# Performance work log

Hardware: AMD Instinct MI355X
Metric: run time of the kernel (lower is better)

Reference implementation:

```python
import jax, jax.numpy as jnp
import numpy as np
import math

HEADS = 16
HIDDEN = 2048
D_K = HIDDEN // HEADS
BATCH = 2
SEQ = 2048
ROPE_THETA = 10000.0


def make_freqs_cis(seq_len, d_k, theta=ROPE_THETA):
    # Llama rotary frequencies; returned as (seq, d_k//2, 2) = (cos, sin)
    inv_freq = 1.0 / (theta ** (np.arange(0, d_k, 2, dtype=np.float32) / d_k))
    t = np.arange(seq_len, dtype=np.float32)
    ang = np.outer(t, inv_freq)  # (seq, d_k//2)
    return jnp.asarray(np.stack([np.cos(ang), np.sin(ang)], axis=-1))


def setup_inputs() -> dict:
    key = jax.random.key(0)
    ks = jax.random.split(key, 5)
    scale = 1.0 / math.sqrt(HIDDEN)
    return {
        "x": jax.random.normal(ks[0], (BATCH, SEQ, HIDDEN), dtype=jnp.float32),
        "freqs_cis": make_freqs_cis(SEQ, D_K),
        "wq": jax.random.normal(ks[1], (HIDDEN, HIDDEN), dtype=jnp.float32) * scale,
        "wk": jax.random.normal(ks[2], (HIDDEN, HIDDEN), dtype=jnp.float32) * scale,
        "wv": jax.random.normal(ks[3], (HIDDEN, HIDDEN), dtype=jnp.float32) * scale,
        "wo": jax.random.normal(ks[4], (HIDDEN, HIDDEN), dtype=jnp.float32) * scale,
    }


def _apply_rope(t, cos, sin):
    # t: (B, S, h, d_k); cos/sin: (1, S, 1, d_k//2)
    B, S, h, dk = t.shape
    tp = t.reshape(B, S, h, dk // 2, 2)
    t0, t1 = tp[..., 0], tp[..., 1]
    r0 = t0 * cos - t1 * sin
    r1 = t0 * sin + t1 * cos
    return jnp.stack([r0, r1], axis=-1).reshape(B, S, h, dk)


def reference(x, freqs_cis, wq, wk, wv, wo):
    B, S, H = x.shape
    h, dk = HEADS, H // HEADS
    # nn.Linear(bias=False): y = x @ W.T
    q = (x @ wq.T).reshape(B, S, h, dk)
    k = (x @ wk.T).reshape(B, S, h, dk)
    v = (x @ wv.T).reshape(B, S, h, dk)
    cos = freqs_cis[None, :, None, :, 0]
    sin = freqs_cis[None, :, None, :, 1]
    q = _apply_rope(q, cos, sin)
    k = _apply_rope(k, cos, sin)
    # (B, h, S, dk)
    q = q.transpose(0, 2, 1, 3)
    k = k.transpose(0, 2, 1, 3)
    v = v.transpose(0, 2, 1, 3)
    scores = jnp.einsum("bhqd,bhkd->bhqk", q, k) / math.sqrt(dk)
    causal = jnp.tril(jnp.ones((S, S), dtype=bool))
    scores = jnp.where(causal[None, None], scores, -jnp.inf)
    attn = jax.nn.softmax(scores, axis=-1)
    out = jnp.einsum("bhqk,bhkd->bhqd", attn, v)
    out = out.transpose(0, 2, 1, 3).reshape(B, S, H)
    return out @ wo.T
```

## Files before the change

kernel.cpp:

```cpp
#include <hip/hip_runtime.h>

#define SEQ 2048
#define HID 2048
#define NH 16
#define DK 128
#define NTOK 4096

typedef __bf16 bf16x8 __attribute__((ext_vector_type(8)));
typedef float f32x4 __attribute__((ext_vector_type(4)));
typedef unsigned int u32x4 __attribute__((ext_vector_type(4)));

__device__ __forceinline__ unsigned short f2bf(float f) {
  unsigned int u = __builtin_bit_cast(unsigned int, f);
  u += 0x7fffu + ((u >> 16) & 1u);
  return (unsigned short)(u >> 16);
}
__device__ __forceinline__ float bf2f(unsigned int lo16) {
  return __builtin_bit_cast(float, lo16 << 16);
}

__device__ __forceinline__ void async_cp16(const void* g, void* l) {
  __builtin_amdgcn_global_load_lds(
      (__attribute__((address_space(1))) void*)const_cast<void*>(g),
      (__attribute__((address_space(3))) void*)l, 16, 0, 0);
}

__global__ void convert_all_kernel(const float* __restrict__ x,
                                   const float* __restrict__ wq,
                                   const float* __restrict__ wk,
                                   const float* __restrict__ wv,
                                   const float* __restrict__ wo,
                                   unsigned short* __restrict__ xb,
                                   unsigned short* __restrict__ wqb,
                                   unsigned short* __restrict__ wkb,
                                   unsigned short* __restrict__ wvb,
                                   unsigned short* __restrict__ wob) {
  const int bid = blockIdx.x;
  const float* src;
  unsigned short* dst;
  int base;
  if (bid < 8192) {
    src = x; dst = xb; base = bid;
  } else {
    const int t = (bid - 8192) >> 12;
    base = (bid - 8192) & 4095;
    src = (t == 0) ? wq : (t == 1) ? wk : (t == 2) ? wv : wo;
    dst = (t == 0) ? wqb : (t == 1) ? wkb : (t == 2) ? wvb : wob;
  }
  const int i = base * 256 + threadIdx.x;
  float4 v = ((const float4*)src)[i];
  ushort4 o;
  o.x = f2bf(v.x); o.y = f2bf(v.y); o.z = f2bf(v.z); o.w = f2bf(v.w);
  ((ushort4*)dst)[i] = o;
}

template<bool F32OUT>
__global__ __launch_bounds__(256, 3)
void gemm_bt_kernel(const unsigned short* __restrict__ A,
                    const unsigned short* __restrict__ B0,
                    const unsigned short* __restrict__ B1,
                    const unsigned short* __restrict__ B2,
                    unsigned short* __restrict__ O0,
                    unsigned short* __restrict__ O1,
                    unsigned short* __restrict__ O2,
                    float* __restrict__ Of,
                    const float* __restrict__ fc) {
  __shared__ alignas(16) unsigned short As[128 * 64];
  __shared__ alignas(16) unsigned short Bs[128 * 64];

  const int bx = blockIdx.x, by = blockIdx.y;
  const unsigned short* B;
  unsigned short* Ob = nullptr;
  int sel = 0, col0;
  if (F32OUT) {
    B = B0;
    col0 = bx * 128;
  } else {
    sel = bx >> 4;
    B = (sel == 0) ? B0 : (sel == 1) ? B1 : B2;
    Ob = (sel == 0) ? O0 : (sel == 1) ? O1 : O2;
    col0 = (bx & 15) * 128;
  }
  const int row0 = by * 128;

  const int tid = threadIdx.x;
  const int wave = tid >> 6, lane = tid & 63;
  const int quad = lane >> 4, r = lane & 15;
  const int wm = wave >> 1, wn = wave & 1;
  const int jbase = wave * 256 + lane;

  f32x4 acc[4][4] = {};

  for (int k0 = 0; k0 < HID; k0 += 64) {
    for (int t = 0; t < 4; ++t) {
      const int j = jbase + t * 64;
      const int m = j >> 3;
      const int gc = (j & 7) ^ (m & 7);
      async_cp16(A + (size_t)(row0 + m) * HID + k0 + gc * 8, As + j * 8);
      async_cp16(B + (size_t)(col0 + m) * HID + k0 + gc * 8, Bs + j * 8);
    }
    __syncthreads();
    for (int kk = 0; kk < 2; ++kk) {
      bf16x8 af[4], bfr[4];
      for (int mt = 0; mt < 4; ++mt) {
        const int m = wm * 64 + mt * 16 + r;
        const int slot = (kk * 4 + quad) ^ (m & 7);
        af[mt] = __builtin_bit_cast(bf16x8, *(const u32x4*)(As + m * 64 + slot * 8));
      }
      for (int nt = 0; nt < 4; ++nt) {
        const int n = wn * 64 + nt * 16 + r;
        const int slot = (kk * 4 + quad) ^ (n & 7);
        bfr[nt] = __builtin_bit_cast(bf16x8, *(const u32x4*)(Bs + n * 64 + slot * 8));
      }
      for (int mt = 0; mt < 4; ++mt)
        for (int nt = 0; nt < 4; ++nt)
          acc[mt][nt] = __builtin_amdgcn_mfma_f32_16x16x32_bf16(
              af[mt], bfr[nt], acc[mt][nt], 0, 0, 0);
    }
    __syncthreads();
  }

  if (!F32OUT && sel == 2) {
    for (int mt = 0; mt < 4; ++mt) {
      const int row = row0 + wm * 64 + mt * 16 + quad * 4;
      const int b = row >> 11, s = row & (SEQ - 1);
      for (int nt = 0; nt < 4; ++nt) {
        const int col = col0 + wn * 64 + nt * 16 + r;
        ushort4 pk;
        pk.x = f2bf(acc[mt][nt][0]);
        pk.y = f2bf(acc[mt][nt][1]);
        pk.z = f2bf(acc[mt][nt][2]);
        pk.w = f2bf(acc[mt][nt][3]);
        *(ushort4*)(Ob + ((size_t)(b * HID + col)) * SEQ + s) = pk;
      }
    }
    return;
  }

  if (!F32OUT) {
    const float qs = (sel == 0) ? 0.08838834764831845f : 1.0f;
    for (int mt = 0; mt < 4; ++mt) {
      const int row = row0 + wm * 64 + mt * 16 + quad * 4;
      for (int nt = 0; nt < 4; ++nt) {
        const int col = col0 + wn * 64 + nt * 16 + r;
        const int d = (wn * 64 + nt * 16 + r) >> 1;
        for (int v = 0; v < 4; ++v) {
          const int s = (row + v) & (SEQ - 1);
          const float2 cs = *(const float2*)(fc + s * 128 + 2 * d);
          const float val = acc[mt][nt][v];
          const float par = __shfl_xor(val, 1, 64);
          const float res = (r & 1) ? (par * cs.y + val * cs.x)
                                    : (val * cs.x - par * cs.y);
          Ob[(size_t)(row + v) * HID + col] = f2bf(res * qs);
        }
      }
    }
    return;
  }

  for (int mt = 0; mt < 4; ++mt) {
    const int row = row0 + wm * 64 + mt * 16 + quad * 4;
    for (int nt = 0; nt < 4; ++nt) {
      const int col = col0 + wn * 64 + nt * 16 + r;
      for (int v = 0; v < 4; ++v)
        Of[(size_t)(row + v) * HID + col] = acc[mt][nt][v];
    }
  }
}

__global__ __launch_bounds__(256, 2)
void flash_attn_kernel(const unsigned short* __restrict__ Qb,
                       const unsigned short* __restrict__ Kb,
                       const unsigned short* __restrict__ VtG,
                       unsigned short* __restrict__ Ob) {
  __shared__ alignas(16) unsigned short KsA[64 * 128];
  __shared__ alignas(16) unsigned short KsB[64 * 128];
  __shared__ alignas(16) unsigned short VsA[128 * 64];
  __shared__ alignas(16) unsigned short VsB[128 * 64];
  __shared__ alignas(16) unsigned short Ps[4][16 * 64];

  const int bx = blockIdx.x, bh = blockIdx.y;
  const int tid = threadIdx.x, wave = tid >> 6, lane = tid & 63;
  const int quad = lane >> 4, r = lane & 15;
  const int tokbase = (bh >> 4) * SEQ;
  const int h = bh & 15;

  const u32x4 onesv = {0x3F803F80u, 0x3F803F80u, 0x3F803F80u, 0x3F803F80u};

  auto stage = [&](int kt, unsigned short* Ks, unsigned short* Vs) {
    for (int t = 0; t < 4; ++t) {
      const int j = t * 256 + tid;
      const int n = j >> 4, slot = j & 15;
      const int gc = (slot & 8) | ((slot & 7) ^ (n & 7));
      async_cp16(Kb + (size_t)(tokbase + kt * 64 + n) * HID + h * DK + gc * 8,
                 Ks + j * 8);
    }
    for (int t = 0; t < 4; ++t) {
      const int j = t * 256 + tid;
      const int d = j >> 3, slot = j & 7;
      const int gc = slot ^ (d & 7);
      async_cp16(VtG + ((size_t)(bh * DK + d)) * SEQ + kt * 64 + gc * 8,
                 Vs + j * 8);
    }
  };

  for (int phase = 0; phase < 2; ++phase) {
    const int qt = phase ? (31 - bx) : bx;
    const int q0 = qt * 64;

    u32x4 qf[4];
    {
      const unsigned short* qrow =
          Qb + (size_t)(tokbase + q0 + wave * 16 + r) * HID + h * DK;
      for (int kk = 0; kk < 4; ++kk)
        qf[kk] = *(const u32x4*)(qrow + kk * 32 + quad * 8);
    }

    f32x4 o[8] = {};
    float m_i[4], l_i[4];
    for (int v = 0; v < 4; ++v) { m_i[v] = -__builtin_inff(); l_i[v] = 0.f; }

    auto body = [&](const unsigned short* Ks, const unsigned short* Vs, int kt) {
      f32x4 s[4];
      for (int nt = 0; nt < 4; ++nt) {
        f32x4 a = {};
        const int n = nt * 16 + r;
        for (int kk = 0; kk < 4; ++kk) {
          const int c = kk * 4 + quad;
          const int slot = (c & 8) | ((c & 7) ^ (r & 7));
          u32x4 bkf = *(const u32x4*)(Ks + n * 128 + slot * 8);
          a = __builtin_amdgcn_mfma_f32_16x16x32_bf16(
              __builtin_bit_cast(bf16x8, qf[kk]),
              __builtin_bit_cast(bf16x8, bkf), a, 0, 0, 0);
        }
        s[nt] = a;
      }

      if (kt == qt) {
        const int qrow_g = q0 + wave * 16 + quad * 4;
        for (int nt = 0; nt < 4; ++nt) {
          const int col = kt * 64 + nt * 16 + r;
          for (int v = 0; v < 4; ++v)
            if (col > qrow_g + v) s[nt][v] = -__builtin_inff();
        }
      }

      float mx[4];
      for (int v = 0; v < 4; ++v)
        mx[v] = fmaxf(fmaxf(s[0][v], s[1][v]), fmaxf(s[2][v], s[3][v]));
      for (int off = 1; off < 16; off <<= 1)
        for (int v = 0; v < 4; ++v)
          mx[v] = fmaxf(mx[v], __shfl_xor(mx[v], off, 64));

      float alpha[4];
      for (int v = 0; v < 4; ++v) {
        const float mnew = fmaxf(m_i[v], mx[v]);
        alpha[v] = __expf(m_i[v] - mnew);
        m_i[v] = mnew;
      }

      unsigned short* ps = &Ps[wave][0];
      for (int nt = 0; nt < 4; ++nt) {
        const int chunk = nt * 2 + (r >> 3);
        for (int v = 0; v < 4; ++v) {
          const float p = __expf(s[nt][v] - m_i[v]);
          const int row = quad * 4 + v;
          const int slot = chunk ^ (row & 7);
          ps[row * 64 + slot * 8 + (r & 7)] = f2bf(p);
        }
      }
      for (int dt = 0; dt < 8; ++dt)
        for (int v = 0; v < 4; ++v)
          o[dt][v] *= alpha[v];
      __asm__ volatile("" ::: "memory");

      f32x4 rsacc = {};
      for (int kk2 = 0; kk2 < 2; ++kk2) {
        const int c = kk2 * 4 + quad;
        const int aslot = c ^ (r & 7);
        u32x4 pa = *(const u32x4*)(ps + r * 64 + aslot * 8);
        rsacc = __builtin_amdgcn_mfma_f32_16x16x32_bf16(
            __builtin_bit_cast(bf16x8, pa),
            __builtin_bit_cast(bf16x8, onesv), rsacc, 0, 0, 0);
        for (int dt = 0; dt < 8; ++dt) {
          const int d = dt * 16 + r;
          const int bslot = c ^ (d & 7);
          u32x4 bv = *(const u32x4*)(Vs + d * 64 + bslot * 8);
          o[dt] = __builtin_amdgcn_mfma_f32_16x16x32_bf16(
              __builtin_bit_cast(bf16x8, pa),
              __builtin_bit_cast(bf16x8, bv), o[dt], 0, 0, 0);
        }
      }
      for (int v = 0; v < 4; ++v)
        l_i[v] = l_i[v] * alpha[v] + rsacc[v];
    };

    stage(0, KsA, VsA);
    int kt = 0;
    while (true) {
      __syncthreads();
      if (kt + 1 <= qt) stage(kt + 1, KsB, VsB);
      body(KsA, VsA, kt);
      if (++kt > qt) break;
      __syncthreads();
      if (kt + 1 <= qt) stage(kt + 1, KsA, VsA);
      body(KsB, VsB, kt);
      if (++kt > qt) break;
    }

    float li[4];
    for (int v = 0; v < 4; ++v) li[v] = 1.f / l_i[v];
    for (int dt = 0; dt < 8; ++dt)
      for (int v = 0; v < 4; ++v) {
        const size_t row = (size_t)tokbase + q0 + wave * 16 + quad * 4 + v;
        Ob[row * HID + h * DK + dt * 16 + r] = f2bf(o[dt][v] * li[v]);
      }
    __syncthreads();
  }
}

extern "C" void kernel_launch(void* const* d_in, const int* in_sizes, int n_in,
                              void* d_out, int out_size, void* d_ws, size_t ws_size,
                              hipStream_t stream) {
  const float* x  = (const float*)d_in[0];
  const float* fc = (const float*)d_in[1];
  const float* wq = (const float*)d_in[2];
  const float* wk = (const float*)d_in[3];
  const float* wv = (const float*)d_in[4];
  const float* wo = (const float*)d_in[5];
  float* out = (float*)d_out;

  unsigned short* xb  = (unsigned short*)d_ws;
  unsigned short* wqb = xb  + (size_t)NTOK * HID;
  unsigned short* wkb = wqb + (size_t)HID * HID;
  unsigned short* wvb = wkb + (size_t)HID * HID;
  unsigned short* wob = wvb + (size_t)HID * HID;
  unsigned short* qb  = wob + (size_t)HID * HID;
  unsigned short* kb  = qb  + (size_t)NTOK * HID;
  unsigned short* vtb = kb  + (size_t)NTOK * HID;
  unsigned short* ab  = vtb + (size_t)NTOK * HID;

  convert_all_kernel<<<8192 + 4 * 4096, 256, 0, stream>>>(
      x, wq, wk, wv, wo, xb, wqb, wkb, wvb, wob);

  gemm_bt_kernel<false><<<dim3(48, 32), 256, 0, stream>>>(
      xb, wqb, wkb, wvb, qb, kb, vtb, nullptr, fc);

  flash_attn_kernel<<<dim3(16, 32), 256, 0, stream>>>(qb, kb, vtb, ab);

  gemm_bt_kernel<true><<<dim3(16, 32), 256, 0, stream>>>(
      ab, wob, nullptr, nullptr, nullptr, nullptr, nullptr, out, fc);
}
```

Baseline: 368.6 us.

## Double-buffer GEMM LDS tiles and pack RoPE table into bf16 pairs

The GEMM kernel now uses two LDS buffers for the A and B tiles, so the async global-to-LDS copy of the next k-tile is issued before the MFMAs on the current tile run. This aims to overlap memory latency with compute, and it drops one barrier per iteration. The doubled shared memory (64 KB per block) forces launch bounds down from 3 to 2 blocks per CU. Separately, the convert kernel packs cos/sin into one bf16 pair per 32-bit word, halving the RoPE table traffic in the epilogue at the cost of precision in the rotation factors.

```diff
diff --git a/kernel.cpp b/kernel.cpp
--- a/kernel.cpp
+++ b/kernel.cpp
@@ -30,12 +30,21 @@
                                    const float* __restrict__ wk,
                                    const float* __restrict__ wv,
                                    const float* __restrict__ wo,
+                                   const float* __restrict__ fc,
                                    unsigned short* __restrict__ xb,
                                    unsigned short* __restrict__ wqb,
                                    unsigned short* __restrict__ wkb,
                                    unsigned short* __restrict__ wvb,
-                                   unsigned short* __restrict__ wob) {
+                                   unsigned short* __restrict__ wob,
+                                   unsigned int* __restrict__ fcb) {
   const int bid = blockIdx.x;
+  if (bid >= 24576) {
+    const int idx = (bid - 24576) * 256 + threadIdx.x;
+    const int s = idx >> 6, d = idx & 63;
+    const float2 cs = *(const float2*)(fc + s * 128 + 2 * d);
+    fcb[idx] = (unsigned int)f2bf(cs.x) | ((unsigned int)f2bf(cs.y) << 16);
+    return;
+  }
   const float* src;
   unsigned short* dst;
   int base;
@@ -55,7 +64,7 @@
 }
 
 template<bool F32OUT>
-__global__ __launch_bounds__(256, 3)
+__global__ __launch_bounds__(256, 2)
 void gemm_bt_kernel(const unsigned short* __restrict__ A,
                     const unsigned short* __restrict__ B0,
                     const unsigned short* __restrict__ B1,
@@ -64,9 +73,11 @@
                     unsigned short* __restrict__ O1,
                     unsigned short* __restrict__ O2,
                     float* __restrict__ Of,
-                    const float* __restrict__ fc) {
-  __shared__ alignas(16) unsigned short As[128 * 64];
-  __shared__ alignas(16) unsigned short Bs[128 * 64];
+                    const unsigned int* __restrict__ fcb) {
+  __shared__ alignas(16) unsigned short As0[128 * 64];
+  __shared__ alignas(16) unsigned short Bs0[128 * 64];
+  __shared__ alignas(16) unsigned short As1[128 * 64];
+  __shared__ alignas(16) unsigned short Bs1[128 * 64];
 
   const int bx = blockIdx.x, by = blockIdx.y;
   const unsigned short* B;
@@ -91,33 +102,49 @@
 
   f32x4 acc[4][4] = {};
 
-  for (int k0 = 0; k0 < HID; k0 += 64) {
+  auto stage = [&](int kt, unsigned short* as, unsigned short* bs) {
+    const int k0 = kt * 64;
     for (int t = 0; t < 4; ++t) {
       const int j = jbase + t * 64;
       const int m = j >> 3;
       const int gc = (j & 7) ^ (m & 7);
-      async_cp16(A + (size_t)(row0 + m) * HID + k0 + gc * 8, As + j * 8);
-      async_cp16(B + (size_t)(col0 + m) * HID + k0 + gc * 8, Bs + j * 8);
-    }
-    __syncthreads();
+      async_cp16(A + (size_t)(row0 + m) * HID + k0 + gc * 8, as + j * 8);
+      async_cp16(B + (size_t)(col0 + m) * HID + k0 + gc * 8, bs + j * 8);
+    }
+  };
+
+  auto body = [&](const unsigned short* as, const unsigned short* bs) {
     for (int kk = 0; kk < 2; ++kk) {
       bf16x8 af[4], bfr[4];
       for (int mt = 0; mt < 4; ++mt) {
         const int m = wm * 64 + mt * 16 + r;
         const int slot = (kk * 4 + quad) ^ (m & 7);
-        af[mt] = __builtin_bit_cast(bf16x8, *(const u32x4*)(As + m * 64 + slot * 8));
+        af[mt] = __builtin_bit_cast(bf16x8, *(const u32x4*)(as + m * 64 + slot * 8));
       }
       for (int nt = 0; nt < 4; ++nt) {
         const int n = wn * 64 + nt * 16 + r;
         const int slot = (kk * 4 + quad) ^ (n & 7);
-        bfr[nt] = __builtin_bit_cast(bf16x8, *(const u32x4*)(Bs + n * 64 + slot * 8));
+        bfr[nt] = __builtin_bit_cast(bf16x8, *(const u32x4*)(bs + n * 64 + slot * 8));
       }
       for (int mt = 0; mt < 4; ++mt)
         for (int nt = 0; nt < 4; ++nt)
           acc[mt][nt] = __builtin_amdgcn_mfma_f32_16x16x32_bf16(
               af[mt], bfr[nt], acc[mt][nt], 0, 0, 0);
     }
+  };
+
+  const int NK = HID / 64;
+  stage(0, As0, Bs0);
+  int kt = 0;
+  while (true) {
     __syncthreads();
+    if (kt + 1 < NK) stage(kt + 1, As1, Bs1);
+    body(As0, Bs0);
+    if (++kt == NK) break;
+    __syncthreads();
+    if (kt + 1 < NK) stage(kt + 1, As0, Bs0);
+    body(As1, Bs1);
+    if (++kt == NK) break;
   }
 
   if (!F32OUT && sel == 2) {
@@ -146,11 +173,12 @@
         const int d = (wn * 64 + nt * 16 + r) >> 1;
         for (int v = 0; v < 4; ++v) {
           const int s = (row + v) & (SEQ - 1);
-          const float2 cs = *(const float2*)(fc + s * 128 + 2 * d);
+          const unsigned int u = fcb[s * 64 + d];
+          const float c = bf2f(u & 0xffffu), sn = bf2f(u >> 16);
           const float val = acc[mt][nt][v];
           const float par = __shfl_xor(val, 1, 64);
-          const float res = (r & 1) ? (par * cs.y + val * cs.x)
-                                    : (val * cs.x - par * cs.y);
+          const float res = (r & 1) ? (par * sn + val * c)
+                                    : (val * c - par * sn);
           Ob[(size_t)(row + v) * HID + col] = f2bf(res * qs);
         }
       }
@@ -339,15 +367,16 @@
   unsigned short* kb  = qb  + (size_t)NTOK * HID;
   unsigned short* vtb = kb  + (size_t)NTOK * HID;
   unsigned short* ab  = vtb + (size_t)NTOK * HID;
-
-  convert_all_kernel<<<8192 + 4 * 4096, 256, 0, stream>>>(
-      x, wq, wk, wv, wo, xb, wqb, wkb, wvb, wob);
+  unsigned int*   fcb = (unsigned int*)(ab + (size_t)NTOK * HID);
+
+  convert_all_kernel<<<24576 + 512, 256, 0, stream>>>(
+      x, wq, wk, wv, wo, fc, xb, wqb, wkb, wvb, wob, fcb);
 
   gemm_bt_kernel<false><<<dim3(48, 32), 256, 0, stream>>>(
-      xb, wqb, wkb, wvb, qb, kb, vtb, nullptr, fc);
+      xb, wqb, wkb, wvb, qb, kb, vtb, nullptr, fcb);
 
   flash_attn_kernel<<<dim3(16, 32), 256, 0, stream>>>(qb, kb, vtb, ab);
 
   gemm_bt_kernel<true><<<dim3(16, 32), 256, 0, stream>>>(
-      ab, wob, nullptr, nullptr, nullptr, nullptr, nullptr, out, fc);
-}
+      ab, wob, nullptr, nullptr, nullptr, nullptr, nullptr, out, fcb);
+}
```

Result: no change. 374.1 us (+1.5%).
